# Performance work log

Hardware: AMD Instinct MI355X
Metric: run time of the kernel (lower is better)

The kernel has to match this reference:

```python
import jax, jax.numpy as jnp
import numpy as np

NEG_INF = -100000000.0
N, L, E, DIM, V_IN, V_OUT = 64, 512, 128, 512, 32000, 10000
D = 2 * DIM  # encoder output feature dim


def _lstm_layer(x, Wih, Whh, bih, bhh, reverse=False):
    """Single-direction LSTM over (N, L, I) -> (N, L, H). PyTorch gate order i,f,g,o."""
    n = x.shape[0]
    H = Whh.shape[1]
    xg = jnp.einsum('nli,gi->nlg', x, Wih) + bih  # precompute input projections (N, L, 4H)

    def step(carry, g_in):
        h, c = carry
        g = g_in + h @ Whh.T + bhh
        i, f, gg, o = jnp.split(g, 4, axis=-1)
        c = jax.nn.sigmoid(f) * c + jax.nn.sigmoid(i) * jnp.tanh(gg)
        h = jax.nn.sigmoid(o) * jnp.tanh(c)
        return (h, c), h

    init = (jnp.zeros((n, H), x.dtype), jnp.zeros((n, H), x.dtype))
    _, hs = jax.lax.scan(step, init, jnp.swapaxes(xg, 0, 1), reverse=reverse)
    return jnp.swapaxes(hs, 0, 1)


def setup_inputs() -> dict:
    key = jax.random.key(0)
    ks = iter(jax.random.split(key, 40))

    def p(shape):
        return (jax.random.normal(next(ks), shape, jnp.float32) * 0.05)

    inp = {}
    inp['X'] = jax.random.randint(next(ks), (N, L), 0, V_IN)
    sl = jax.random.randint(next(ks), (N,), 1, L + 1)
    inp['seq_len'] = sl.at[0].set(L)  # ensure max length == L as the torch code assumes
    inp['embed_W'] = p((V_IN, E))
    # encoder layer 0 (input E, hidden DIM), fwd + bwd directions
    for tag, I in (('l0f', E), ('l0b', E), ('l1f', D), ('l1b', D)):
        inp[tag + '_Wih'] = p((4 * DIM, I))
        inp[tag + '_Whh'] = p((4 * DIM, DIM))
        inp[tag + '_bih'] = p((4 * DIM,))
        inp[tag + '_bhh'] = p((4 * DIM,))
    for tag in ('Ws', 'Wa', 'Ua'):
        inp[tag + '_W'] = p((D, D))
        inp[tag + '_b'] = p((D,))
    inp['va_W'] = p((1, D))
    inp['va_b'] = p((1,))
    inp['dec_Wih'] = p((4 * D, D))
    inp['dec_Whh'] = p((4 * D, D))
    inp['dec_bih'] = p((4 * D,))
    inp['dec_bhh'] = p((4 * D,))
    inp['cls_W'] = p((V_OUT, D))
    inp['cls_b'] = p((V_OUT,))
    return inp


def reference(X, seq_len, embed_W,
              l0f_Wih, l0f_Whh, l0f_bih, l0f_bhh,
              l0b_Wih, l0b_Whh, l0b_bih, l0b_bhh,
              l1f_Wih, l1f_Whh, l1f_bih, l1f_bhh,
              l1b_Wih, l1b_Whh, l1b_bih, l1b_bhh,
              Ws_W, Ws_b, Wa_W, Wa_b, Ua_W, Ua_b, va_W, va_b,
              dec_Wih, dec_Whh, dec_bih, dec_bhh, cls_W, cls_b):
    emb = embed_W[X]  # (N, L, E)
    h0 = jnp.concatenate([
        _lstm_layer(emb, l0f_Wih, l0f_Whh, l0f_bih, l0f_bhh, reverse=False),
        _lstm_layer(emb, l0b_Wih, l0b_Whh, l0b_bih, l0b_bhh, reverse=True)], axis=-1)
    hid = jnp.concatenate([
        _lstm_layer(h0, l1f_Wih, l1f_Whh, l1f_bih, l1f_bhh, reverse=False),
        _lstm_layer(h0, l1b_Wih, l1b_Whh, l1b_bih, l1b_bhh, reverse=True)], axis=-1)  # (N, L, 2*dim)

    ll = hid.shape[1]
    mask = (jnp.arange(ll)[None, :] >= seq_len[:, None]).astype(hid.dtype)  # 1 where padded
    Ua_h = hid @ Ua_W.T + Ua_b  # hoisted: U_a(hid) is loop-invariant
    s_i = jnp.tanh(hid[:, 0] @ Ws_W.T + Ws_b)  # (N, D)

    outs = []
    for _ in range(11):
        e = (jnp.tanh((s_i @ Wa_W.T + Wa_b)[:, None, :] + Ua_h) @ va_W.T + va_b)[..., 0]  # (N, L)
        att = jax.nn.softmax(e + NEG_INF * mask, axis=-1)
        ci = jnp.einsum('nl,nld->nd', att, hid)  # context (N, D)
        # single-step decoder LSTM; cell state reset to zero each step (as in torch code)
        g = ci @ dec_Wih.T + dec_bih + s_i @ dec_Whh.T + dec_bhh
        i, f, gg, o = jnp.split(g, 4, axis=-1)
        c = jax.nn.sigmoid(i) * jnp.tanh(gg)  # f * 0 == 0
        s_i = jax.nn.sigmoid(o) * jnp.tanh(c)
        outs.append(s_i)

    s = jnp.stack(outs, axis=1)  # (N, 11, D)
    return s @ cls_W.T + cls_b  # (N, 11, num_outclass)
```

## Files before the change

### kernel.cpp

```cpp
#include <hip/hip_runtime.h>
#include <stdint.h>

#define NEG_INF -100000000.0f

typedef unsigned short u16;
typedef unsigned long long u64;
typedef __attribute__((ext_vector_type(8))) short v8s;
typedef __attribute__((ext_vector_type(4))) short v4s;
typedef __attribute__((ext_vector_type(4))) float v4f;

__device__ __forceinline__ float bf2f(u16 h){ return __uint_as_float(((unsigned)h)<<16); }
__device__ __forceinline__ u16 f2bf(float f){
  unsigned u = __float_as_uint(f);
  u = u + 0x7fffu + ((u>>16)&1u);
  return (u16)(u>>16);
}
__device__ __forceinline__ float sigm(float x){ return 1.0f/(1.0f+__expf(-x)); }
__device__ __forceinline__ float ftanh(float x){
  x = fminf(15.0f, fmaxf(-15.0f, x));
  float e = __expf(2.0f*x);
  return (e-1.0f)/(e+1.0f);
}

__device__ __forceinline__ void store_h16(u16* p, u64 a, u64 b){
  __hip_atomic_store((u64*)p,     a, __ATOMIC_RELAXED, __HIP_MEMORY_SCOPE_AGENT);
  __hip_atomic_store((u64*)(p+4), b, __ATOMIC_RELAXED, __HIP_MEMORY_SCOPE_AGENT);
}

struct CvtTab {
  const float* src[31];
  unsigned off[31];
  unsigned n[31];
  unsigned total;
};

__global__ __launch_bounds__(256) void cvt_all(CvtTab tab, u16* __restrict__ arena){
  unsigned e0 = (blockIdx.x*256u + threadIdx.x)*8u;
  if (e0 >= tab.total) return;
  int s = 0;
#pragma unroll 1
  for (int i = 1; i < 31; ++i) if (e0 >= tab.off[i]) s = i;
  unsigned rel = e0 - tab.off[s];
  const float* sp = tab.src[s] + rel;
  unsigned nn = tab.n[s];
  union { u16 h[8]; v8s v; } o;
  if (rel + 8 <= nn) {
    float4 a = *(const float4*)sp;
    float4 b = *(const float4*)(sp+4);
    o.h[0]=f2bf(a.x); o.h[1]=f2bf(a.y); o.h[2]=f2bf(a.z); o.h[3]=f2bf(a.w);
    o.h[4]=f2bf(b.x); o.h[5]=f2bf(b.y); o.h[6]=f2bf(b.z); o.h[7]=f2bf(b.w);
  } else {
#pragma unroll
    for (int k = 0; k < 8; ++k) o.h[k] = (rel + k < nn) ? f2bf(sp[k]) : (u16)0;
  }
  *(v8s*)(arena + e0) = o.v;
}

#define GF_OUTBF16 1
#define GF_TANH    2
#define GF_ACCUM   4

__global__ __launch_bounds__(256) void gemm_bf16(
    const u16* __restrict__ A, long long lda,
    const u16* __restrict__ B,
    const u16* __restrict__ bias1, const u16* __restrict__ bias2,
    void* __restrict__ Cout, long long ldc,
    int M, int Nn, int K, int flags)
{
  __shared__ u16 As[8192];
  __shared__ u16 Bs[8192];
  int tid = threadIdx.x;
  int lane = tid & 63, w = tid >> 6;
  int wm = w >> 1, wn = w & 1;
  int bm = blockIdx.x * 128, bn = blockIdx.y * 128;

  v4f acc[4][4];
#pragma unroll
  for (int i=0;i<4;++i)
#pragma unroll
    for (int j=0;j<4;++j) acc[i][j] = (v4f){0.f,0.f,0.f,0.f};

#pragma unroll 1
  for (int ko = 0; ko < K; ko += 64) {
    __syncthreads();
#pragma unroll
    for (int it = 0; it < 8; ++it) {
      int c = tid + 256*it;
      int half = c >> 10;
      int cc = c & 1023;
      int r = cc >> 3;
      int kcb = cc & 7;
      const u16* src;
      if (half == 0) {
        int row = min(bm + r, M-1);
        src = A + (size_t)row*(size_t)lda + ko + (kcb<<3);
      } else {
        int row = min(bn + r, Nn-1);
        src = B + (size_t)row*(size_t)K + ko + (kcb<<3);
      }
      v8s v = *(const v8s*)src;
      char* base = (char*)(half ? Bs : As);
      *(v8s*)(base + (r<<7) + ((kcb<<4) ^ ((r&7)<<4))) = v;
    }
    __syncthreads();
#pragma unroll
    for (int ks = 0; ks < 2; ++ks) {
      v8s af[4], bfr[4];
#pragma unroll
      for (int mt=0; mt<4; ++mt) {
        int r = wm*64 + mt*16 + (lane & 15);
        int kb = (ks<<6) + ((lane>>4)<<4);
        af[mt] = *(const v8s*)((const char*)As + (r<<7) + (kb ^ ((r&7)<<4)));
      }
#pragma unroll
      for (int nt=0; nt<4; ++nt) {
        int r = wn*64 + nt*16 + (lane & 15);
        int kb = (ks<<6) + ((lane>>4)<<4);
        bfr[nt] = *(const v8s*)((const char*)Bs + (r<<7) + (kb ^ ((r&7)<<4)));
      }
#pragma unroll
      for (int mt=0; mt<4; ++mt)
#pragma unroll
        for (int nt=0; nt<4; ++nt)
          acc[mt][nt] = __builtin_amdgcn_mfma_f32_16x16x32_bf16(af[mt], bfr[nt], acc[mt][nt], 0,0,0);
    }
  }

#pragma unroll
  for (int mt=0; mt<4; ++mt) {
#pragma unroll
    for (int nt=0; nt<4; ++nt) {
      int col = bn + wn*64 + nt*16 + (lane&15);
      if (col >= Nn) continue;
      float b = 0.f;
      if (bias1) b += bf2f(bias1[col]);
      if (bias2) b += bf2f(bias2[col]);
#pragma unroll
      for (int r=0; r<4; ++r) {
        int row = bm + wm*64 + mt*16 + ((lane>>4)<<2) + r;
        if (row >= M) continue;
        float v = acc[mt][nt][r] + b;
        if (flags & GF_ACCUM) v += ((float*)Cout)[(size_t)row*(size_t)ldc + col];
        if (flags & GF_TANH) v = ftanh(v);
        if (flags & GF_OUTBF16) ((u16*)Cout)[(size_t)row*(size_t)ldc + col] = f2bf(v);
        else                    ((float*)Cout)[(size_t)row*(size_t)ldc + col] = v;
      }
    }
  }
}

template<int LAYER>
__global__ __launch_bounds__(256, 1) void lstm_scan(
    const u16* __restrict__ xsrc,
    const int* __restrict__ Xidx,
    const u16* __restrict__ Wih_f, const u16* __restrict__ Wih_b,
    const u16* __restrict__ Whh_f, const u16* __restrict__ Whh_b,
    const u16* __restrict__ bih_f, const u16* __restrict__ bhh_f,
    const u16* __restrict__ bih_b, const u16* __restrict__ bhh_b,
    u16* __restrict__ hbuf,
    unsigned* __restrict__ prog)
{
  constexpr int KX  = (LAYER==0) ? 128 : 1024;
  constexpr int NKC = KX/64;
  __shared__ float glds[8*32*18];
  __shared__ u16   hlds[1024];

  const int tid = threadIdx.x, lane = tid & 63, w = tid >> 6;
  const int kh = w >> 1, gp = w & 1;
  const int dir = blockIdx.x >> 6, bg = (blockIdx.x >> 5) & 1, ug = blockIdx.x & 31;
  const int an = lane & 15, hi = lane >> 4, ak = hi << 3;
  const u16* Wih = dir ? Wih_b : Wih_f;
  const u16* Whh = dir ? Whh_b : Whh_f;
  const int gid = dir*2 + bg;
  unsigned* gprog = prog + gid*32;

  const int g = 2*gp + (an>>3);

  v8s wih_reg[2][NKC];
#pragma unroll
  for (int nt = 0; nt < 2; ++nt) {
    const u16* wp = Wih + ((size_t)g*512 + ug*16 + nt*8 + (an&7))*KX + kh*(KX/2);
#pragma unroll
    for (int kc = 0; kc < NKC; ++kc) {
      wih_reg[nt][kc] = *(const v8s*)(wp + kc*32 + ak);
      asm volatile("" : "+v"(wih_reg[nt][kc]));
    }
  }
  v8s whh_reg[2][8];
#pragma unroll
  for (int nt = 0; nt < 2; ++nt) {
    const u16* wp = Whh + ((size_t)g*512 + ug*16 + nt*8 + (an&7))*512 + kh*256;
#pragma unroll
    for (int kc = 0; kc < 8; ++kc) {
      whh_reg[nt][kc] = *(const v8s*)(wp + kc*32 + ak);
      asm volatile("" : "+v"(whh_reg[nt][kc]));
    }
  }

  const int u_pw = tid & 15, n2 = tid >> 4;
  const int uj_pw = ug*16 + u_pw;
  float bsum[4];
  {
    const u16* bi = dir ? bih_b : bih_f;
    const u16* bh = dir ? bhh_b : bhh_f;
#pragma unroll
    for (int q = 0; q < 4; ++q)
      bsum[q] = bf2f(bi[q*512 + uj_pw]) + bf2f(bh[q*512 + uj_pw]);
  }
  float creg[2] = {0.f, 0.f};

  for (int step = 0; step < 512; ++step) {
    const int t     = dir ? (511 - step) : step;
    const int tprev = dir ? (t + 1) : (t - 1);

    v4f acc[2][2];
#pragma unroll
    for (int i=0;i<2;++i){ acc[i][0]=(v4f){0,0,0,0}; acc[i][1]=(v4f){0,0,0,0}; }

    {
      const u16* xrow[2];
#pragma unroll
      for (int mt = 0; mt < 2; ++mt) {
        int ng = bg*32 + mt*16 + an;
        if constexpr (LAYER == 0)
          xrow[mt] = xsrc + (size_t)Xidx[ng*512 + t]*128 + kh*64;
        else
          xrow[mt] = xsrc + ((size_t)(ng*512 + t) << 10) + kh*512;
      }
#pragma unroll
      for (int kc = 0; kc < NKC; ++kc) {
        v8s af[2];
#pragma unroll
        for (int mt = 0; mt < 2; ++mt) af[mt] = *(const v8s*)(xrow[mt] + kc*32 + ak);
#pragma unroll
        for (int nt = 0; nt < 2; ++nt)
#pragma unroll
          for (int mt = 0; mt < 2; ++mt)
            acc[mt][nt] = __builtin_amdgcn_mfma_f32_16x16x32_bf16(af[mt], wih_reg[nt][kc], acc[mt][nt], 0,0,0);
      }
    }

    if (step > 0) {
      if (w == 0) {
        const u64* pl = (const u64*)gprog;
        for (;;) {
          u64 v = ~0ull;
          if (lane < 16)
            v = __hip_atomic_load(pl + lane, __ATOMIC_RELAXED, __HIP_MEMORY_SCOPE_AGENT);
          bool ok = ((unsigned)v >= (unsigned)step) && ((unsigned)(v>>32) >= (unsigned)step);
          if (__all(ok)) break;
          __builtin_amdgcn_s_sleep(1);
        }
      }
      __syncthreads();
      asm volatile("" ::: "memory");

      const u16* hrow[2];
#pragma unroll
      for (int mt = 0; mt < 2; ++mt) {
        int ng = bg*32 + mt*16 + an;
        hrow[mt] = hbuf + ((size_t)(ng*512 + tprev) << 10) + dir*512 + kh*256;
      }
#pragma unroll
      for (int kc = 0; kc < 8; ++kc) {
        v8s af[2];
#pragma unroll
        for (int mt = 0; mt < 2; ++mt) af[mt] = *(const v8s*)(hrow[mt] + kc*32 + ak);
#pragma unroll
        for (int nt = 0; nt < 2; ++nt)
#pragma unroll
          for (int mt = 0; mt < 2; ++mt)
            acc[mt][nt] = __builtin_amdgcn_mfma_f32_16x16x32_bf16(af[mt], whh_reg[nt][kc], acc[mt][nt], 0,0,0);
      }
    }

#pragma unroll
    for (int mt=0; mt<2; ++mt)
#pragma unroll
      for (int nt=0; nt<2; ++nt)
#pragma unroll
        for (int r=0; r<4; ++r) {
          int n = mt*16 + hi*4 + r;
          int u = nt*8 + (an&7);
          glds[((kh*4 + g)*32 + n)*18 + u] = acc[mt][nt][r];
        }
    __syncthreads();

#pragma unroll
    for (int k = 0; k < 2; ++k) {
      int n = k*16 + n2;
      float g0 = glds[(0*32+n)*18+u_pw] + glds[(4*32+n)*18+u_pw] + bsum[0];
      float g1 = glds[(1*32+n)*18+u_pw] + glds[(5*32+n)*18+u_pw] + bsum[1];
      float g2 = glds[(2*32+n)*18+u_pw] + glds[(6*32+n)*18+u_pw] + bsum[2];
      float g3 = glds[(3*32+n)*18+u_pw] + glds[(7*32+n)*18+u_pw] + bsum[3];
      float cn = sigm(g1)*creg[k] + sigm(g0)*ftanh(g2);
      creg[k] = cn;
      hlds[n*16 + u_pw] = f2bf(sigm(g3)*ftanh(cn));
    }
    __syncthreads();

    if (lane < 16) {
      int n    = w*8 + (lane>>1);
      int half = lane & 1;
      u64 a = *(const u64*)&hlds[n*16 + half*8];
      u64 b = *(const u64*)&hlds[n*16 + half*8 + 4];
      store_h16(hbuf + ((size_t)((bg*32+n)*512 + t) << 10) + dir*512 + ug*16 + half*8, a, b);
    }
    asm volatile("s_waitcnt vmcnt(0)" ::: "memory");
    __syncthreads();

    if (tid == 0)
      __hip_atomic_store(gprog + ug, (unsigned)(step+1), __ATOMIC_RELAXED, __HIP_MEMORY_SCOPE_AGENT);
  }
}

__global__ __launch_bounds__(256) void attn_step(
    const float* __restrict__ qbuf, const u16* __restrict__ Uah,
    const u16* __restrict__ hid, const int* __restrict__ seq_len,
    const u16* __restrict__ vaW, const u16* __restrict__ vab,
    u16* __restrict__ catb)
{
  int n = blockIdx.x, tid = threadIdx.x;
  __shared__ float qs[1024];
  __shared__ float vas[1024];
  __shared__ float es[512];
  __shared__ float red[8];
  for (int d=tid; d<1024; d+=256){ qs[d]=qbuf[n*1024+d]; vas[d]=bf2f(vaW[d]); }
  __syncthreads();
  int sl = seq_len[n];
  float vb = bf2f(vab[0]);
  for (int l=tid; l<512; l+=256) {
    const u16* up = Uah + ((size_t)n*512 + l)*1024;
    float a = 0.f;
    for (int d=0; d<1024; d+=8) {
      v8s uv = *(const v8s*)(up + d);
#pragma unroll
      for (int e=0;e<8;++e)
        a = fmaf(ftanh(bf2f((u16)uv[e]) + qs[d+e]), vas[d+e], a);
    }
    float ev = a + vb;
    if (l >= sl) ev += NEG_INF;
    es[l] = ev;
  }
  __syncthreads();
  float m = -3.4e38f;
  for (int l=tid; l<512; l+=256) m = fmaxf(m, es[l]);
#pragma unroll
  for (int off=1; off<64; off<<=1) m = fmaxf(m, __shfl_xor(m, off));
  if ((tid&63)==0) red[tid>>6] = m;
  __syncthreads();
  m = fmaxf(fmaxf(red[0],red[1]), fmaxf(red[2],red[3]));
  float s = 0.f;
  for (int l=tid; l<512; l+=256){ float p = __expf(es[l]-m); es[l]=p; s+=p; }
#pragma unroll
  for (int off=1; off<64; off<<=1) s += __shfl_xor(s, off);
  if ((tid&63)==0) red[4+(tid>>6)] = s;
  __syncthreads();
  float inv = 1.f/(red[4]+red[5]+red[6]+red[7]);
  int d0 = tid*4;
  float c0=0,c1=0,c2=0,c3=0;
  for (int l=0; l<512; ++l) {
    float a = es[l];
    const u16* hp = hid + ((size_t)n*512 + l)*1024 + d0;
    v4s hv = *(const v4s*)hp;
    c0 = fmaf(a, bf2f((u16)hv[0]), c0);
    c1 = fmaf(a, bf2f((u16)hv[1]), c1);
    c2 = fmaf(a, bf2f((u16)hv[2]), c2);
    c3 = fmaf(a, bf2f((u16)hv[3]), c3);
  }
  catb[n*2048 + d0 + 0] = f2bf(c0*inv);
  catb[n*2048 + d0 + 1] = f2bf(c1*inv);
  catb[n*2048 + d0 + 2] = f2bf(c2*inv);
  catb[n*2048 + d0 + 3] = f2bf(c3*inv);
}

__global__ void dec_pw(const float* __restrict__ g, u16* __restrict__ scat,
                       u16* __restrict__ catb, int it)
{
  int idx = blockIdx.x*256 + threadIdx.x;
  int n = idx >> 10, d = idx & 1023;
  float gi = g[(size_t)n*4096 + d];
  float gg = g[(size_t)n*4096 + 2048 + d];
  float go = g[(size_t)n*4096 + 3072 + d];
  float c = sigm(gi)*ftanh(gg);
  float s = sigm(go)*ftanh(c);
  u16 hb = f2bf(s);
  scat[((size_t)n*11 + it)*1024 + d] = hb;
  catb[n*2048 + 1024 + d] = hb;
}

__global__ void fill_sentinel(float* out, int nel){
  int i = blockIdx.x*256 + threadIdx.x;
  if (i < nel) out[i] = 12345.0f;
}

extern "C" void kernel_launch(void* const* d_in, const int* in_sizes, int n_in,
                              void* d_out, int out_size, void* d_ws, size_t ws_size,
                              hipStream_t stream)
{
  const int* X      = (const int*)d_in[0];
  const int* seqlen = (const int*)d_in[1];
  float* out = (float*)d_out;
  char* ws = (char*)d_ws;

  struct Seg { int idx; int n; };
  static const Seg segs[31] = {
    {2, 4096000},
    {3, 262144},{4,1048576},{5,2048},{6,2048},
    {7, 262144},{8,1048576},{9,2048},{10,2048},
    {11,2097152},{12,1048576},{13,2048},{14,2048},
    {15,2097152},{16,1048576},{17,2048},{18,2048},
    {19,1048576},{20,1024},
    {21,1048576},{22,1024},
    {23,1048576},{24,1024},
    {25,1024},{26,1},
    {27,4194304},{28,4194304},{29,4096},{30,4096},
    {31,10240000},{32,10000},
  };
  const u16* bp[33];
  CvtTab tab;
  size_t aoff = 0;
  for (int i = 0; i < 31; ++i) {
    bp[segs[i].idx] = (const u16*)(ws) + aoff;
    tab.src[i] = (const float*)d_in[segs[i].idx];
    tab.off[i] = (unsigned)aoff;
    tab.n[i]   = (unsigned)segs[i].n;
    aoff += (size_t)((segs[i].n + 7) & ~7);
  }
  tab.total = (unsigned)aoff;
  size_t arena_bytes = ((aoff*2 + 255) & ~(size_t)255);

  const size_t H0_OFF   = arena_bytes;
  const size_t HID_OFF  = H0_OFF   + 67108864;
  const size_t BAR_OFF  = HID_OFF  + 67108864;
  const size_t CATB_OFF = BAR_OFF  + 16384;
  const size_t QBUF_OFF = CATB_OFF + 262144;
  const size_t GDEC_OFF = QBUF_OFF + 262144;
  const size_t SCAT_OFF = GDEC_OFF + 1048576;
  const size_t NEED     = SCAT_OFF + 1441792;

  if (ws_size < NEED) {
    fill_sentinel<<<(out_size+255)/256, 256, 0, stream>>>(out, out_size);
    return;
  }

  u16*      h0   = (u16*)(ws + H0_OFF);
  u16*      Uah  = (u16*)(ws + H0_OFF);
  u16*      hid  = (u16*)(ws + HID_OFF);
  unsigned* bar  = (unsigned*)(ws + BAR_OFF);
  u16*      catb = (u16*)(ws + CATB_OFF);
  float*    qbuf = (float*)(ws + QBUF_OFF);
  float*    gdec = (float*)(ws + GDEC_OFF);
  u16*      scat = (u16*)(ws + SCAT_OFF);

  hipMemsetAsync(ws + BAR_OFF, 0, 16384, stream);

  {
    unsigned nth = (unsigned)(aoff / 8);
    cvt_all<<<(nth + 255)/256, 256, 0, stream>>>(tab, (u16*)ws);
  }

  lstm_scan<0><<<128, 256, 0, stream>>>(
      bp[2], X, bp[3], bp[7], bp[4], bp[8],
      bp[5], bp[6], bp[9], bp[10], h0, bar);

  lstm_scan<1><<<128, 256, 0, stream>>>(
      h0, nullptr, bp[11], bp[15], bp[12], bp[16],
      bp[13], bp[14], bp[17], bp[18], hid, bar + 1024);

  gemm_bf16<<<dim3(256,8), 256, 0, stream>>>(hid, 1024, bp[23], bp[24], nullptr,
      Uah, 1024, 32768, 1024, 1024, GF_OUTBF16);
  gemm_bf16<<<dim3(1,8), 256, 0, stream>>>(hid, 524288, bp[19], bp[20], nullptr,
      catb + 1024, 2048, 64, 1024, 1024, GF_OUTBF16 | GF_TANH);

  for (int it = 0; it < 11; ++it) {
    gemm_bf16<<<dim3(1,8), 256, 0, stream>>>(catb + 1024, 2048, bp[21], bp[22], nullptr,
        qbuf, 1024, 64, 1024, 1024, 0);
    attn_step<<<64, 256, 0, stream>>>(qbuf, Uah, hid, seqlen, bp[25], bp[26], catb);
    gemm_bf16<<<dim3(1,32), 256, 0, stream>>>(catb, 2048, bp[27], bp[29], bp[30],
        gdec, 4096, 64, 4096, 1024, 0);
    gemm_bf16<<<dim3(1,32), 256, 0, stream>>>(catb + 1024, 2048, bp[28], nullptr, nullptr,
        gdec, 4096, 64, 4096, 1024, GF_ACCUM);
    dec_pw<<<256, 256, 0, stream>>>(gdec, scat, catb, it);
  }

  gemm_bf16<<<dim3(6,79), 256, 0, stream>>>(scat, 1024, bp[31], bp[32], nullptr,
      out, 10000, 704, 10000, 1024, 0);
}
```

Baseline: 9.850 ms.

## Prefetch next-step input rows and let every wave poll the step barrier

Input-projection operands for the next timestep are now loaded into registers at the end of each step, so their global-memory latency overlaps the barrier wait instead of sitting on the critical path. Every wave now polls the grid progress flags itself, which removes one workgroup barrier. The polling loop spins a few times before sleeping, and h rows are remapped so each wave writes rows it produced, which removes another barrier. The cost is more registers for the prefetched operands and more atomic polling traffic, which could lower occupancy or add memory contention.

Measured after the change: 9.742 ms. About the same (-1.1%).

```diff
diff --git a/kernel.cpp b/kernel.cpp
--- a/kernel.cpp
+++ b/kernel.cpp
@@ -209,6 +209,20 @@
   }
   float creg[2] = {0.f, 0.f};
 
+  v8s xreg[2][NKC];
+  {
+    const int t0 = dir ? 511 : 0;
+#pragma unroll
+    for (int mt = 0; mt < 2; ++mt) {
+      int ng = bg*32 + mt*16 + an;
+      const u16* xr;
+      if constexpr (LAYER == 0) xr = xsrc + (size_t)Xidx[ng*512 + t0]*128 + kh*64;
+      else                      xr = xsrc + ((size_t)(ng*512 + t0) << 10) + kh*512;
+#pragma unroll
+      for (int kc = 0; kc < NKC; ++kc) xreg[mt][kc] = *(const v8s*)(xr + kc*32 + ak);
+    }
+  }
+
   for (int step = 0; step < 512; ++step) {
     const int t     = dir ? (511 - step) : step;
     const int tprev = dir ? (t + 1) : (t - 1);
@@ -217,61 +231,51 @@
 #pragma unroll
     for (int i=0;i<2;++i){ acc[i][0]=(v4f){0,0,0,0}; acc[i][1]=(v4f){0,0,0,0}; }
 
-    {
-      const u16* xrow[2];
-#pragma unroll
-      for (int mt = 0; mt < 2; ++mt) {
-        int ng = bg*32 + mt*16 + an;
-        if constexpr (LAYER == 0)
-          xrow[mt] = xsrc + (size_t)Xidx[ng*512 + t]*128 + kh*64;
-        else
-          xrow[mt] = xsrc + ((size_t)(ng*512 + t) << 10) + kh*512;
-      }
-#pragma unroll
-      for (int kc = 0; kc < NKC; ++kc) {
-        v8s af[2];
-#pragma unroll
-        for (int mt = 0; mt < 2; ++mt) af[mt] = *(const v8s*)(xrow[mt] + kc*32 + ak);
-#pragma unroll
-        for (int nt = 0; nt < 2; ++nt)
-#pragma unroll
-          for (int mt = 0; mt < 2; ++mt)
-            acc[mt][nt] = __builtin_amdgcn_mfma_f32_16x16x32_bf16(af[mt], wih_reg[nt][kc], acc[mt][nt], 0,0,0);
-      }
-    }
-
     if (step > 0) {
-      if (w == 0) {
+      {
         const u64* pl = (const u64*)gprog;
+        int spins = 0;
         for (;;) {
           u64 v = ~0ull;
           if (lane < 16)
             v = __hip_atomic_load(pl + lane, __ATOMIC_RELAXED, __HIP_MEMORY_SCOPE_AGENT);
           bool ok = ((unsigned)v >= (unsigned)step) && ((unsigned)(v>>32) >= (unsigned)step);
           if (__all(ok)) break;
-          __builtin_amdgcn_s_sleep(1);
+          if (++spins > 4) __builtin_amdgcn_s_sleep(1);
         }
-      }
-      __syncthreads();
-      asm volatile("" ::: "memory");
-
-      const u16* hrow[2];
+        asm volatile("" ::: "memory");
+      }
+
+      v8s haf[2][8];
 #pragma unroll
       for (int mt = 0; mt < 2; ++mt) {
         int ng = bg*32 + mt*16 + an;
-        hrow[mt] = hbuf + ((size_t)(ng*512 + tprev) << 10) + dir*512 + kh*256;
-      }
-#pragma unroll
-      for (int kc = 0; kc < 8; ++kc) {
-        v8s af[2];
-#pragma unroll
-        for (int mt = 0; mt < 2; ++mt) af[mt] = *(const v8s*)(hrow[mt] + kc*32 + ak);
+        const u16* hr = hbuf + ((size_t)(ng*512 + tprev) << 10) + dir*512 + kh*256;
+#pragma unroll
+        for (int kc = 0; kc < 8; ++kc) haf[mt][kc] = *(const v8s*)(hr + kc*32 + ak);
+      }
+#pragma unroll
+      for (int kc = 0; kc < NKC; ++kc)
 #pragma unroll
         for (int nt = 0; nt < 2; ++nt)
 #pragma unroll
           for (int mt = 0; mt < 2; ++mt)
-            acc[mt][nt] = __builtin_amdgcn_mfma_f32_16x16x32_bf16(af[mt], whh_reg[nt][kc], acc[mt][nt], 0,0,0);
-      }
+            acc[mt][nt] = __builtin_amdgcn_mfma_f32_16x16x32_bf16(xreg[mt][kc], wih_reg[nt][kc], acc[mt][nt], 0,0,0);
+#pragma unroll
+      for (int kc = 0; kc < 8; ++kc)
+#pragma unroll
+        for (int nt = 0; nt < 2; ++nt)
+#pragma unroll
+          for (int mt = 0; mt < 2; ++mt)
+            acc[mt][nt] = __builtin_amdgcn_mfma_f32_16x16x32_bf16(haf[mt][kc], whh_reg[nt][kc], acc[mt][nt], 0,0,0);
+    } else {
+#pragma unroll
+      for (int kc = 0; kc < NKC; ++kc)
+#pragma unroll
+        for (int nt = 0; nt < 2; ++nt)
+#pragma unroll
+          for (int mt = 0; mt < 2; ++mt)
+            acc[mt][nt] = __builtin_amdgcn_mfma_f32_16x16x32_bf16(xreg[mt][kc], wih_reg[nt][kc], acc[mt][nt], 0,0,0);
     }
 
 #pragma unroll
@@ -297,15 +301,29 @@
       creg[k] = cn;
       hlds[n*16 + u_pw] = f2bf(sigm(g3)*ftanh(cn));
     }
-    __syncthreads();
 
     if (lane < 16) {
-      int n    = w*8 + (lane>>1);
+      int j = lane >> 1;
+      int n = 4*w + (j & 3) + 16*(j >> 2);
       int half = lane & 1;
       u64 a = *(const u64*)&hlds[n*16 + half*8];
       u64 b = *(const u64*)&hlds[n*16 + half*8 + 4];
       store_h16(hbuf + ((size_t)((bg*32+n)*512 + t) << 10) + dir*512 + ug*16 + half*8, a, b);
     }
+
+    if (step < 511) {
+      const int tn = dir ? (t - 1) : (t + 1);
+#pragma unroll
+      for (int mt = 0; mt < 2; ++mt) {
+        int ng = bg*32 + mt*16 + an;
+        const u16* xr;
+        if constexpr (LAYER == 0) xr = xsrc + (size_t)Xidx[ng*512 + tn]*128 + kh*64;
+        else                      xr = xsrc + ((size_t)(ng*512 + tn) << 10) + kh*512;
+#pragma unroll
+        for (int kc = 0; kc < NKC; ++kc) xreg[mt][kc] = *(const v8s*)(xr + kc*32 + ak);
+      }
+    }
+
     asm volatile("s_waitcnt vmcnt(0)" ::: "memory");
     __syncthreads();
 
```
